# Kernel optimization log

Hardware: AMD Instinct MI355X
Metric: run time of the kernel (lower is better)

The kernel has to match this reference:

```python
import jax, jax.numpy as jnp
import numpy as np

N_NODES = 50000
N_EDGES = 800000
STALK_DIM = 16
N_TYPES = 16


def setup_inputs() -> dict:
    key = jax.random.key(0)
    k1, k2, k3, k4 = jax.random.split(key, 4)
    entity_reps = jax.random.normal(k1, (STALK_DIM, N_NODES), dtype=jnp.float32)
    restriction_maps = jax.random.normal(k2, (N_TYPES, N_TYPES, STALK_DIM, STALK_DIM), dtype=jnp.float32)
    edge_index = jax.random.randint(k3, (2, N_EDGES), 0, N_NODES, dtype=jnp.int64 if jax.config.jax_enable_x64 else jnp.int32).astype(jnp.int32)
    entity_types = jax.random.randint(k4, (N_NODES,), 0, N_TYPES).astype(jnp.int32)
    return {"entity_reps": entity_reps, "restriction_maps": restriction_maps,
            "edge_index": edge_index, "entity_types": entity_types}


def reference(entity_reps, restriction_maps, edge_index, entity_types):
    src, dst = edge_index[0], edge_index[1]
    n_nodes = entity_reps.shape[1]

    # deg^{-1/2} from in-degree on dst (col), inf -> 0 for isolated nodes
    deg = jax.ops.segment_sum(jnp.ones_like(src, dtype=entity_reps.dtype), dst,
                              num_segments=n_nodes)
    inv_deg = jnp.where(deg > 0, jax.lax.rsqrt(jnp.maximum(deg, 1.0)), 0.0)

    # normalized reps: x @ diag(inv_deg)  -> scale each node column
    x = entity_reps * inv_deg[None, :]            # [d, n_nodes]

    t_src = entity_types[src]                     # [E]
    t_dst = entity_types[dst]
    head_maps = restriction_maps[t_src, t_dst]    # [E, d, d]
    tail_maps = restriction_maps[t_dst, t_src]    # [E, d, d]

    x_src = x[:, src].T                           # [E, d]
    x_dst = x[:, dst].T                           # [E, d]
    head_emb = jnp.einsum('eij,ej->ei', head_maps, x_src)  # [E, d]
    tail_emb = jnp.einsum('eij,ej->ei', tail_maps, x_dst)  # [E, d]

    # scatter-add head at src, subtract tail at dst
    comparison = (jax.ops.segment_sum(head_emb, src, num_segments=n_nodes)
                  - jax.ops.segment_sum(tail_emb, dst, num_segments=n_nodes))  # [n_nodes, d]

    # sum over d of ||comparison[:, j]||^2 == total sum of squares
    return jnp.sum(comparison * comparison)
```

## Files before the change

kernel.cpp:

```cpp
#include <hip/hip_runtime.h>

constexpr int NNODES_C = 50000;
constexpr int D = 16;
constexpr int NT = 16;
constexpr int E_C = 800000;

constexpr int NODE_P = 128;
constexpr int NPART  = 391;
constexpr int CHUNK  = 1024;
constexpr int NBLK   = 782;
constexpr int SLOT   = 24;
constexpr int CAP_E  = NBLK * SLOT;
constexpr int CNT_PITCH = 784;

constexpr size_t OFF_ENT   = 0;
constexpr size_t OFF_CNT   = (size_t)NPART * CAP_E * 2;
constexpr size_t FAST_NEED = OFF_CNT + (size_t)NPART * CNT_PITCH * 4;

constexpr size_t F_TCNT  = 3200000;
constexpr size_t F_TLIST = 3200064;



__device__ __forceinline__ void emit_edge(unsigned int s, unsigned int d,
                                          unsigned int ts, unsigned int td,
                                          unsigned int* cur,
                                          unsigned short* entries) {
    const unsigned int ps = atomicAdd(&cur[s >> 7], 1u);
    entries[ps] = (unsigned short)(((s & 127u) << 5) | td);
    const unsigned int pd = atomicAdd(&cur[d >> 7], 1u);
    entries[pd] = (unsigned short)(((d & 127u) << 5) | 0x10u | ts);
}

__global__ __launch_bounds__(256)
void scatter_kernel(const int* __restrict__ ei, const int* __restrict__ types,
                    unsigned short* __restrict__ entries,
                    unsigned int* __restrict__ cnt_g,
                    float* __restrict__ out, int E) {
    __shared__ unsigned int cur[NPART];
    const int tid = threadIdx.x;
    const int b   = blockIdx.x;
    if (b == 0 && tid == 0) out[0] = 0.0f;
    for (int p = tid; p < NPART; p += 256)
        cur[p] = (unsigned int)p * CAP_E + (unsigned int)b * SLOT;
    __syncthreads();

    const int start = b * CHUNK;
    const int end   = min(start + CHUNK, E);
    const int e0    = start + tid * 4;

    if (e0 + 3 < end) {
        const int4 s4 = *reinterpret_cast<const int4*>(ei + e0);
        const int4 d4 = *reinterpret_cast<const int4*>(ei + E + e0);
        const unsigned int ss[4] = {(unsigned int)s4.x, (unsigned int)s4.y,
                                    (unsigned int)s4.z, (unsigned int)s4.w};
        const unsigned int dd[4] = {(unsigned int)d4.x, (unsigned int)d4.y,
                                    (unsigned int)d4.z, (unsigned int)d4.w};
        unsigned int ts[4], td[4];
        #pragma unroll
        for (int k = 0; k < 4; ++k) { ts[k] = (unsigned int)types[ss[k]];
                                      td[k] = (unsigned int)types[dd[k]]; }
        #pragma unroll
        for (int k = 0; k < 4; ++k)
            emit_edge(ss[k], dd[k], ts[k], td[k], cur, entries);
    } else if (e0 < end) {
        for (int e = e0; e < end; ++e) {
            const unsigned int s  = (unsigned int)ei[e];
            const unsigned int d  = (unsigned int)ei[E + e];
            emit_edge(s, d, (unsigned int)types[s], (unsigned int)types[d],
                      cur, entries);
        }
    }
    __syncthreads();
    for (int p = tid; p < NPART; p += 256)
        cnt_g[p * CNT_PITCH + b] =
            cur[p] - ((unsigned int)p * CAP_E + (unsigned int)b * SLOT);
}

__global__ __launch_bounds__(512)
void hist_node_kernel(const float* __restrict__ reps,
                      const float* __restrict__ rmaps,
                      const unsigned short* __restrict__ entries,
                      const unsigned int* __restrict__ cnt_g,
                      const int* __restrict__ types,
                      float* __restrict__ out, int N) {
    __shared__ unsigned int  hist[NODE_P * 17];
    __shared__ float         C[NODE_P][16];
    __shared__ float         X[NODE_P][16];
    __shared__ unsigned char llist[NT * NODE_P];
    __shared__ float         IDG[NODE_P];
    __shared__ int           lcnt[NT];
    __shared__ unsigned int  cnt_s[NBLK];
    __shared__ float         wpart[8];

    const int tid = threadIdx.x;
    const int p   = blockIdx.x;
    const int n0  = p * NODE_P;
    const int nn  = min(NODE_P, N - n0);

    for (int i = tid; i < NODE_P * 17; i += 512) hist[i] = 0u;
    if (tid < NT) lcnt[tid] = 0;
    for (int i = tid; i < NBLK; i += 512)
        cnt_s[i] = cnt_g[p * CNT_PITCH + i];
    __syncthreads();

    for (int sb = tid; sb < NBLK; sb += 512) {
        const unsigned int cnt = cnt_s[sb];
        if (cnt == 0) continue;
        const uint4* src = reinterpret_cast<const uint4*>(
            entries + ((size_t)p * NBLK + sb) * SLOT);
        const int nch = (int)((cnt + 7) >> 3);
        for (int c = 0; c < nch; ++c) {
            const uint4 v = src[c];
            const unsigned int words[4] = {v.x, v.y, v.z, v.w};
            const unsigned int base = (unsigned int)c * 8;
            #pragma unroll
            for (int k = 0; k < 4; ++k) {
                #pragma unroll
                for (int h = 0; h < 2; ++h) {
                    const unsigned int idx = base + k * 2 + h;
                    if (idx < cnt) {
                        const unsigned int e = (words[k] >> (h * 16)) & 0xFFFFu;
                        atomicAdd(&hist[(e >> 5) * 17 + (e & 15u)],
                                  (e & 0x10u) ? 0x10000u : 1u);
                    }
                }
            }
        }
    }
    {
        const int rg = tid >> 7;
        const int tt = tid & 127;
        if (tt < nn) {
            #pragma unroll
            for (int j = 0; j < 4; ++j)
                X[tt][rg * 4 + j] = reps[(rg * 4 + j) * N + n0 + tt];
        }
    }
    __syncthreads();

    if (tid < nn) {
        unsigned int deg = 0;
        #pragma unroll
        for (int t = 0; t < NT; ++t) deg += (hist[tid * 17 + t] >> 16);
        #pragma unroll
        for (int t = 0; t < NT; ++t) {
            const unsigned int hw = hist[tid * 17 + t];
            C[tid][t] = (float)((int)(hw & 0xFFFFu) - (int)(hw >> 16));
        }
        IDG[tid] = (deg > 0) ? (1.0f / (float)deg) : 0.0f;
        const int ty = types[n0 + tid];
        const int rk = atomicAdd(&lcnt[ty], 1);
        llist[ty * NODE_P + rk] = (unsigned char)tid;
    }
    __syncthreads();

    const int wv = tid >> 6;
    const int l  = tid & 63;
    const int tg = l >> 4;
    const int r  = l & 15;

    float part = 0.0f;
    for (int ty = wv * 2; ty < wv * 2 + 2; ++ty) {
        const int m = lcnt[ty];
        if (m == 0) continue;

        float4 Rf[4][4];
        const float* Rbase = rmaps + (((size_t)ty * NT + tg * 4) * D + r) * D;
        #pragma unroll
        for (int jt = 0; jt < 4; ++jt)
            #pragma unroll
            for (int q = 0; q < 4; ++q)
                Rf[jt][q] = *reinterpret_cast<const float4*>(Rbase + jt * D * D + q * 4);

        for (int idx = 0; idx < m; ++idx) {
            const int nl = llist[ty * NODE_P + idx];
            const float4 x0 = *reinterpret_cast<const float4*>(&X[nl][0]);
            const float4 x1 = *reinterpret_cast<const float4*>(&X[nl][4]);
            const float4 x2 = *reinterpret_cast<const float4*>(&X[nl][8]);
            const float4 x3 = *reinterpret_cast<const float4*>(&X[nl][12]);
            const float4 c4 = *reinterpret_cast<const float4*>(&C[nl][tg * 4]);
            const float idg = IDG[nl];
            const float ca[4] = {c4.x, c4.y, c4.z, c4.w};

            float y = 0.0f;
            #pragma unroll
            for (int jt = 0; jt < 4; ++jt) {
                float s = 0.0f;
                s = fmaf(Rf[jt][0].x, x0.x, s); s = fmaf(Rf[jt][0].y, x0.y, s);
                s = fmaf(Rf[jt][0].z, x0.z, s); s = fmaf(Rf[jt][0].w, x0.w, s);
                s = fmaf(Rf[jt][1].x, x1.x, s); s = fmaf(Rf[jt][1].y, x1.y, s);
                s = fmaf(Rf[jt][1].z, x1.z, s); s = fmaf(Rf[jt][1].w, x1.w, s);
                s = fmaf(Rf[jt][2].x, x2.x, s); s = fmaf(Rf[jt][2].y, x2.y, s);
                s = fmaf(Rf[jt][2].z, x2.z, s); s = fmaf(Rf[jt][2].w, x2.w, s);
                s = fmaf(Rf[jt][3].x, x3.x, s); s = fmaf(Rf[jt][3].y, x3.y, s);
                s = fmaf(Rf[jt][3].z, x3.z, s); s = fmaf(Rf[jt][3].w, x3.w, s);
                y = fmaf(ca[jt], s, y);
            }
            y += __shfl_xor(y, 16);
            y += __shfl_xor(y, 32);
            if (l < 16) part = fmaf(y * y, idg, part);
        }
    }

    #pragma unroll
    for (int off = 32; off > 0; off >>= 1)
        part += __shfl_down(part, off);
    if (l == 0) wpart[wv] = part;
    __syncthreads();
    if (tid == 0) {
        float v = 0.0f;
        #pragma unroll
        for (int i = 0; i < 8; ++i) v += wpart[i];
        if (v != 0.0f) atomicAdd(out, v);
    }
}


__global__ __launch_bounds__(256)
void edge_kernel(const int* __restrict__ ei, const int* __restrict__ types,
                 unsigned int* __restrict__ pk, int E) {
    const int i = (blockIdx.x * blockDim.x + threadIdx.x) * 4;
    if (i >= E) return;
    if (i + 3 < E) {
        const int4 s4 = *reinterpret_cast<const int4*>(ei + i);
        const int4 t4 = *reinterpret_cast<const int4*>(ei + E + i);
        const int ss[4] = {s4.x, s4.y, s4.z, s4.w};
        const int tt[4] = {t4.x, t4.y, t4.z, t4.w};
        #pragma unroll
        for (int k = 0; k < 4; ++k) {
            atomicAdd(&pk[ss[k] * NT + types[tt[k]]], 1u);
            atomicAdd(&pk[tt[k] * NT + types[ss[k]]], 0x10000u);
        }
    } else {
        for (int e = i; e < E; ++e) {
            const int s = ei[e];
            const int t = ei[E + e];
            atomicAdd(&pk[s * NT + types[t]], 1u);
            atomicAdd(&pk[t * NT + types[s]], 0x10000u);
        }
    }
}

__global__ __launch_bounds__(256)
void list_kernel(const int* __restrict__ types,
                 int* __restrict__ tcnt, int* __restrict__ tlist, int N) {
    __shared__ int lcnt[NT];
    __shared__ int lbase[NT];
    if (threadIdx.x < NT) lcnt[threadIdx.x] = 0;
    __syncthreads();
    const int n = blockIdx.x * 256 + threadIdx.x;
    int ty = 0, lr = 0;
    const bool valid = (n < N);
    if (valid) {
        ty = types[n];
        lr = atomicAdd(&lcnt[ty], 1);
    }
    __syncthreads();
    if (threadIdx.x < NT)
        lbase[threadIdx.x] = atomicAdd(&tcnt[threadIdx.x], lcnt[threadIdx.x]);
    __syncthreads();
    if (valid)
        tlist[ty * NNODES_C + lbase[ty] + lr] = n;
}

__global__ __launch_bounds__(256)
void node_kernel(const float* __restrict__ reps,
                 const float* __restrict__ rmaps,
                 const unsigned int* __restrict__ pk,
                 const int* __restrict__ tcnt,
                 const int* __restrict__ tlist,
                 float* __restrict__ out, int N) {
    const int ty  = blockIdx.y;
    const int cnt = tcnt[ty];
    if ((int)(blockIdx.x * 64) >= cnt) return;

    const int tid = threadIdx.x;
    const int w   = tid >> 6;
    const int l   = tid & 63;
    const int tg  = l >> 4;
    const int r   = l & 15;

    float4 Rf[4][4];
    {
        const float* Rbase = rmaps + (((size_t)ty * NT + tg * 4) * D + r) * D;
        #pragma unroll
        for (int jt = 0; jt < 4; ++jt)
            #pragma unroll
            for (int q = 0; q < 4; ++q)
                Rf[jt][q] = *reinterpret_cast<const float4*>(Rbase + jt * D * D + q * 4);
    }

    __shared__ int   NI[64];
    __shared__ float X[64][16];
    __shared__ float C[64][16];
    __shared__ int   PD[64][4];
    __shared__ float IDG[64];

    float part = 0.0f;

    for (int base = blockIdx.x * 64; base < cnt; base += gridDim.x * 64) {
        const int nb = min(64, cnt - base);

        __syncthreads();
        if (tid < nb) NI[tid] = tlist[ty * NNODES_C + base + tid];
        __syncthreads();

        const int b = tid >> 2, q = tid & 3;
        if (b < nb) {
            const int n = NI[b];
            const uint4 pw = reinterpret_cast<const uint4*>(pk + (size_t)n * NT)[q];
            const unsigned int ws4[4] = {pw.x, pw.y, pw.z, pw.w};
            int hsum = 0;
            #pragma unroll
            for (int j = 0; j < 4; ++j) {
                const int hi = (int)(ws4[j] >> 16);
                const int lo = (int)(ws4[j] & 0xFFFFu);
                C[b][q * 4 + j] = (float)(lo - hi);
                hsum += hi;
            }
            PD[b][q] = hsum;
            #pragma unroll
            for (int j = 0; j < 4; ++j)
                X[b][q * 4 + j] = reps[(q * 4 + j) * N + n];
        }
        __syncthreads();
        if (tid < nb) {
            const int dg = PD[tid][0] + PD[tid][1] + PD[tid][2] + PD[tid][3];
            IDG[tid] = (dg > 0) ? (1.0f / (float)dg) : 0.0f;
        }
        __syncthreads();

        for (int bb = w; bb < nb; bb += 4) {
            const float4 x0 = *reinterpret_cast<const float4*>(&X[bb][0]);
            const float4 x1 = *reinterpret_cast<const float4*>(&X[bb][4]);
            const float4 x2 = *reinterpret_cast<const float4*>(&X[bb][8]);
            const float4 x3 = *reinterpret_cast<const float4*>(&X[bb][12]);
            const float4 c4 = *reinterpret_cast<const float4*>(&C[bb][tg * 4]);
            const float idg = IDG[bb];
            const float ca[4] = {c4.x, c4.y, c4.z, c4.w};

            float y = 0.0f;
            #pragma unroll
            for (int jt = 0; jt < 4; ++jt) {
                float s = 0.0f;
                s = fmaf(Rf[jt][0].x, x0.x, s); s = fmaf(Rf[jt][0].y, x0.y, s);
                s = fmaf(Rf[jt][0].z, x0.z, s); s = fmaf(Rf[jt][0].w, x0.w, s);
                s = fmaf(Rf[jt][1].x, x1.x, s); s = fmaf(Rf[jt][1].y, x1.y, s);
                s = fmaf(Rf[jt][1].z, x1.z, s); s = fmaf(Rf[jt][1].w, x1.w, s);
                s = fmaf(Rf[jt][2].x, x2.x, s); s = fmaf(Rf[jt][2].y, x2.y, s);
                s = fmaf(Rf[jt][2].z, x2.z, s); s = fmaf(Rf[jt][2].w, x2.w, s);
                s = fmaf(Rf[jt][3].x, x3.x, s); s = fmaf(Rf[jt][3].y, x3.y, s);
                s = fmaf(Rf[jt][3].z, x3.z, s); s = fmaf(Rf[jt][3].w, x3.w, s);
                y = fmaf(ca[jt], s, y);
            }
            y += __shfl_xor(y, 16);
            y += __shfl_xor(y, 32);
            if (l < 16) part = fmaf(y * y, idg, part);
        }
    }

    #pragma unroll
    for (int off = 32; off > 0; off >>= 1)
        part += __shfl_down(part, off);
    __shared__ float wpart[4];
    if (l == 0) wpart[w] = part;
    __syncthreads();
    if (tid == 0) {
        const float v = wpart[0] + wpart[1] + wpart[2] + wpart[3];
        if (v != 0.0f) atomicAdd(out, v);
    }
}

extern "C" void kernel_launch(void* const* d_in, const int* in_sizes, int n_in,
                              void* d_out, int out_size, void* d_ws, size_t ws_size,
                              hipStream_t stream) {
    const float* reps  = (const float*)d_in[0];
    const float* rmaps = (const float*)d_in[1];
    const int*   ei    = (const int*)d_in[2];
    const int*   types = (const int*)d_in[3];
    float* out = (float*)d_out;

    const int E = in_sizes[2] / 2;
    const int N = in_sizes[3];

    char* ws = (char*)d_ws;
    const bool fast = (N == NNODES_C && E == E_C && ws_size >= FAST_NEED);

    if (fast) {
        unsigned short* entries = (unsigned short*)(ws + OFF_ENT);
        unsigned int*   cnt_g   = (unsigned int*)(ws + OFF_CNT);

        scatter_kernel  <<<NBLK,  256, 0, stream>>>(ei, types, entries, cnt_g, out, E);
        hist_node_kernel<<<NPART, 512, 0, stream>>>(reps, rmaps, entries, cnt_g,
                                                    types, out, N);
    } else {
        unsigned int* pk = (unsigned int*)ws;
        int* tcnt  = (int*)(ws + F_TCNT);
        int* tlist = (int*)(ws + F_TLIST);

        hipMemsetAsync(d_ws, 0, F_TLIST, stream);
        hipMemsetAsync(d_out, 0, sizeof(float), stream);
        edge_kernel<<<(E / 4 + 255) / 256, 256, 0, stream>>>(ei, types, pk, E);
        list_kernel<<<(N + 255) / 256, 256, 0, stream>>>(types, tcnt, tlist, N);
        dim3 grid(52, NT);
        node_kernel<<<grid, 256, 0, stream>>>(reps, rmaps, pk, tcnt, tlist, out, N);
    }
}
```

Before: 44.18 us.

## Stage scatter entries in LDS and write block-major layout with coalesced stores

The scatter kernel now buckets each block's edge entries into a shared-memory staging buffer and then copies the whole staged region to global memory with contiguous 16-byte stores. The global entry and count arrays change from partition-major to block-major layout, and the consumer kernel's indexing is updated to match. This replaces scattered 2-byte global writes with coalesced bulk stores. The cost is that the consumer's reads become strided across blocks, and the scatter kernel uses more LDS. The histogram increment select is also replaced with a shift.

```diff
diff --git a/kernel.cpp b/kernel.cpp
--- a/kernel.cpp
+++ b/kernel.cpp
@@ -10,39 +10,28 @@
 constexpr int CHUNK  = 1024;
 constexpr int NBLK   = 782;
 constexpr int SLOT   = 24;
-constexpr int CAP_E  = NBLK * SLOT;
-constexpr int CNT_PITCH = 784;
+constexpr int BLK_E  = NPART * SLOT;
 
 constexpr size_t OFF_ENT   = 0;
-constexpr size_t OFF_CNT   = (size_t)NPART * CAP_E * 2;
-constexpr size_t FAST_NEED = OFF_CNT + (size_t)NPART * CNT_PITCH * 4;
+constexpr size_t OFF_CNT   = (size_t)NBLK * BLK_E * 2;
+constexpr size_t FAST_NEED = OFF_CNT + (size_t)NBLK * NPART * 4;
 
 constexpr size_t F_TCNT  = 3200000;
 constexpr size_t F_TLIST = 3200064;
 
 
-
-__device__ __forceinline__ void emit_edge(unsigned int s, unsigned int d,
-                                          unsigned int ts, unsigned int td,
-                                          unsigned int* cur,
-                                          unsigned short* entries) {
-    const unsigned int ps = atomicAdd(&cur[s >> 7], 1u);
-    entries[ps] = (unsigned short)(((s & 127u) << 5) | td);
-    const unsigned int pd = atomicAdd(&cur[d >> 7], 1u);
-    entries[pd] = (unsigned short)(((d & 127u) << 5) | 0x10u | ts);
-}
 
 __global__ __launch_bounds__(256)
 void scatter_kernel(const int* __restrict__ ei, const int* __restrict__ types,
                     unsigned short* __restrict__ entries,
                     unsigned int* __restrict__ cnt_g,
                     float* __restrict__ out, int E) {
-    __shared__ unsigned int cur[NPART];
+    __shared__ unsigned short stage[BLK_E];
+    __shared__ unsigned int   cur[NPART];
     const int tid = threadIdx.x;
     const int b   = blockIdx.x;
     if (b == 0 && tid == 0) out[0] = 0.0f;
-    for (int p = tid; p < NPART; p += 256)
-        cur[p] = (unsigned int)p * CAP_E + (unsigned int)b * SLOT;
+    for (int p = tid; p < NPART; p += 256) cur[p] = 0;
     __syncthreads();
 
     const int start = b * CHUNK;
@@ -61,20 +50,35 @@
         for (int k = 0; k < 4; ++k) { ts[k] = (unsigned int)types[ss[k]];
                                       td[k] = (unsigned int)types[dd[k]]; }
         #pragma unroll
-        for (int k = 0; k < 4; ++k)
-            emit_edge(ss[k], dd[k], ts[k], td[k], cur, entries);
+        for (int k = 0; k < 4; ++k) {
+            const unsigned int ps = atomicAdd(&cur[ss[k] >> 7], 1u);
+            stage[(ss[k] >> 7) * SLOT + ps] =
+                (unsigned short)(((ss[k] & 127u) << 5) | td[k]);
+            const unsigned int pd = atomicAdd(&cur[dd[k] >> 7], 1u);
+            stage[(dd[k] >> 7) * SLOT + pd] =
+                (unsigned short)(((dd[k] & 127u) << 5) | 0x10u | ts[k]);
+        }
     } else if (e0 < end) {
         for (int e = e0; e < end; ++e) {
-            const unsigned int s  = (unsigned int)ei[e];
-            const unsigned int d  = (unsigned int)ei[E + e];
-            emit_edge(s, d, (unsigned int)types[s], (unsigned int)types[d],
-                      cur, entries);
-        }
-    }
-    __syncthreads();
-    for (int p = tid; p < NPART; p += 256)
-        cnt_g[p * CNT_PITCH + b] =
-            cur[p] - ((unsigned int)p * CAP_E + (unsigned int)b * SLOT);
+            const unsigned int s = (unsigned int)ei[e];
+            const unsigned int d = (unsigned int)ei[E + e];
+            const unsigned int ps = atomicAdd(&cur[s >> 7], 1u);
+            stage[(s >> 7) * SLOT + ps] =
+                (unsigned short)(((s & 127u) << 5) | (unsigned int)types[d]);
+            const unsigned int pd = atomicAdd(&cur[d >> 7], 1u);
+            stage[(d >> 7) * SLOT + pd] =
+                (unsigned short)(((d & 127u) << 5) | 0x10u | (unsigned int)types[s]);
+        }
+    }
+    __syncthreads();
+
+    {
+        const uint4* sg  = reinterpret_cast<const uint4*>(stage);
+        uint4*       dst = reinterpret_cast<uint4*>(entries + (size_t)b * BLK_E);
+        for (int i = tid; i < BLK_E / 8; i += 256) dst[i] = sg[i];
+        unsigned int* cdst = cnt_g + (size_t)b * NPART;
+        for (int p = tid; p < NPART; p += 256) cdst[p] = cur[p];
+    }
 }
 
 __global__ __launch_bounds__(512)
@@ -101,14 +105,14 @@
     for (int i = tid; i < NODE_P * 17; i += 512) hist[i] = 0u;
     if (tid < NT) lcnt[tid] = 0;
     for (int i = tid; i < NBLK; i += 512)
-        cnt_s[i] = cnt_g[p * CNT_PITCH + i];
+        cnt_s[i] = cnt_g[(size_t)i * NPART + p];
     __syncthreads();
 
     for (int sb = tid; sb < NBLK; sb += 512) {
         const unsigned int cnt = cnt_s[sb];
         if (cnt == 0) continue;
         const uint4* src = reinterpret_cast<const uint4*>(
-            entries + ((size_t)p * NBLK + sb) * SLOT);
+            entries + (size_t)sb * BLK_E + p * SLOT);
         const int nch = (int)((cnt + 7) >> 3);
         for (int c = 0; c < nch; ++c) {
             const uint4 v = src[c];
@@ -122,7 +126,7 @@
                     if (idx < cnt) {
                         const unsigned int e = (words[k] >> (h * 16)) & 0xFFFFu;
                         atomicAdd(&hist[(e >> 5) * 17 + (e & 15u)],
-                                  (e & 0x10u) ? 0x10000u : 1u);
+                                  1u << (e & 0x10u));
                     }
                 }
             }
```

After: 43.77 us. Within noise of the previous version (-0.9%).
